# Kernel tuning notes

Measured on AMD Instinct MI355X. Metric: run time of the kernel, lower is better.

The kernel has to match this reference:

```python
import jax, jax.numpy as jnp
import numpy as np

TEMPERATURE = 0.07


def setup_inputs() -> dict:
    key = jax.random.key(0)
    k1, k2, k3 = jax.random.split(key, 3)
    b, num_proposals, num_phrases, f = 128, 100, 16, 512
    img_features = jax.random.normal(k1, (b, num_proposals, f), dtype=jnp.float32)
    text_features = jax.random.normal(k2, (b, num_phrases, f), dtype=jnp.float32)
    labels = jax.random.randint(k3, (b, b), 0, 2, dtype=jnp.int64)
    return {"img_features": img_features, "text_features": text_features, "labels": labels}


def reference(img_features, text_features, labels):
    # att_matrix[b,d,t,i] = <text[b,t,:], img[d,i,:]>
    att_matrix = jnp.einsum('btf,dif->bdti', text_features, img_features)
    argmax_box = att_matrix.max(axis=3)        # [b, d, t]  max over proposals
    score_matrix = argmax_box.mean(axis=2)     # [b, d]     mean over phrases
    score_exp = jnp.exp(score_matrix / TEMPERATURE)
    return score_exp
```

## Files before the change

kernel.cpp:

```cpp
#include <hip/hip_runtime.h>
#include <hip/hip_bf16.h>
#include <stdint.h>


typedef __attribute__((ext_vector_type(4))) int   v4i;
typedef __attribute__((ext_vector_type(8))) int   v8i;
typedef __attribute__((ext_vector_type(4))) float f32x4;

constexpr int Bb = 128;
constexpr int P  = 100;
constexpr int T  = 16;
constexpr int F  = 512;
constexpr float TEMP = 0.07f;

constexpr int BM = 128;
constexpr int BP = 112;
constexpr int BK = 128;
constexpr int NK = F / BK;
constexpr int NXCD = 8;

__global__ void cvt_kernel(const float4* __restrict__ img, const float4* __restrict__ txt,
                           uint32_t* __restrict__ imgb, uint32_t* __restrict__ txtb,
                           int nimg4, int ntxt4) {
  const int stride = gridDim.x * blockDim.x;
  for (int i = blockIdx.x * blockDim.x + threadIdx.x; i < nimg4; i += stride) {
    float4 v = img[i];
    int w = __builtin_amdgcn_cvt_pk_fp8_f32(v.x, v.y, 0, false);
    w     = __builtin_amdgcn_cvt_pk_fp8_f32(v.z, v.w, w, true);
    imgb[i] = (uint32_t)w;
  }
  for (int i = blockIdx.x * blockDim.x + threadIdx.x; i < ntxt4; i += stride) {
    float4 v = txt[i];
    int w = __builtin_amdgcn_cvt_pk_fp8_f32(v.x, v.y, 0, false);
    w     = __builtin_amdgcn_cvt_pk_fp8_f32(v.z, v.w, w, true);
    txtb[i] = (uint32_t)w;
  }
}

template<bool FUSED>
__global__ __launch_bounds__(256, 3)
void score_kernel(const void* __restrict__ imgp, const void* __restrict__ txtp,
                  float* __restrict__ out) {
  __shared__ __align__(16) unsigned char As[BM * BK];
  __shared__ __align__(16) unsigned char Bs[BP * BK];
  __shared__ float red[BM][2];

  const int L    = blockIdx.x;
  const int xcd  = L & (NXCD - 1);
  const int slot = L >> 3;
  const int d    = xcd * 16 + (slot >> 4);
  const int b0   = (slot & 15) * (BM / T);

  const int tid  = threadIdx.x;
  const int lane = tid & 63;
  const int w    = tid >> 6;
  const int q    = lane >> 4;
  const int n    = lane & 15;
  const int mh   = w & 1;
  const int nh   = w >> 1;

  f32x4 acc[4][4] = {};

  auto stage = [&](int kk) {
    if constexpr (!FUSED) {
      const uint8_t* gi = (const uint8_t*)imgp;
      const uint8_t* gt = (const uint8_t*)txtp;
      const int sub = lane >> 3;
      const int col = (((lane & 7) ^ sub) & 7) * 16;
      #pragma unroll
      for (int rr = 0; rr < 4; rr++) {
        const int c   = rr * 4 + w;
        const int row = c * 8 + sub;
        const uint8_t* ga = gt + (size_t)(b0 * T + row) * F + kk + col;
        __builtin_amdgcn_global_load_lds(
            (const __attribute__((address_space(1))) void*)ga,
            (__attribute__((address_space(3))) void*)&As[c * 1024], 16, 0, 0);
        if (c < BP / 8) {
          const int prow = row < P ? row : 0;
          const uint8_t* gb = gi + ((size_t)d * P + prow) * F + kk + col;
          __builtin_amdgcn_global_load_lds(
              (const __attribute__((address_space(1))) void*)gb,
              (__attribute__((address_space(3))) void*)&Bs[c * 1024], 16, 0, 0);
        }
      }
    } else {
      const float* gi = (const float*)imgp;
      const float* gt = (const float*)txtp;
      #pragma unroll
      for (int s = 0; s < 8; s++) {
        const int slot2 = s * 256 + tid;
        const int row   = slot2 >> 4;
        const int half  = slot2 & 15;
        const int colf  = half * 8;
        const int swz   = ((half >> 1) ^ (row & 7));
        const int offb  = row * BK + swz * 16 + (half & 1) * 8;
        float4 v0 = *(const float4*)(gt + (size_t)(b0 * T + row) * F + kk + colf);
        float4 v1 = *(const float4*)(gt + (size_t)(b0 * T + row) * F + kk + colf + 4);
        int w0 = __builtin_amdgcn_cvt_pk_fp8_f32(v0.x, v0.y, 0, false);
        w0     = __builtin_amdgcn_cvt_pk_fp8_f32(v0.z, v0.w, w0, true);
        int w1 = __builtin_amdgcn_cvt_pk_fp8_f32(v1.x, v1.y, 0, false);
        w1     = __builtin_amdgcn_cvt_pk_fp8_f32(v1.z, v1.w, w1, true);
        *(uint2*)&As[offb] = make_uint2((uint32_t)w0, (uint32_t)w1);
        if (row < BP) {
          const int prow = row < P ? row : 0;
          float4 u0 = *(const float4*)(gi + ((size_t)d * P + prow) * F + kk + colf);
          float4 u1 = *(const float4*)(gi + ((size_t)d * P + prow) * F + kk + colf + 4);
          int x0 = __builtin_amdgcn_cvt_pk_fp8_f32(u0.x, u0.y, 0, false);
          x0     = __builtin_amdgcn_cvt_pk_fp8_f32(u0.z, u0.w, x0, true);
          int x1 = __builtin_amdgcn_cvt_pk_fp8_f32(u1.x, u1.y, 0, false);
          x1     = __builtin_amdgcn_cvt_pk_fp8_f32(u1.z, u1.w, x1, true);
          *(uint2*)&Bs[offb] = make_uint2((uint32_t)x0, (uint32_t)x1);
        }
      }
    }
  };

  const int s0 = (2 * q) ^ (n & 7);
  const int NCT = (BP / 16) - nh * 4;

  #pragma unroll
  for (int k4 = 0; k4 < NK; k4++) {
    stage(k4 * BK);
    __syncthreads();

    v8i a[4];
    #pragma unroll
    for (int rt = 0; rt < 4; rt++) {
      const int off = (mh * 64 + rt * 16 + n) * BK;
      v4i lo = *(const v4i*)&As[off + s0 * 16];
      v4i hi = *(const v4i*)&As[off + (s0 ^ 1) * 16];
      a[rt] = __builtin_shufflevector(lo, hi, 0, 1, 2, 3, 4, 5, 6, 7);
    }
    #pragma unroll
    for (int ct = 0; ct < 4; ct++) {
      if (ct < NCT) {
        const int off = (nh * 64 + ct * 16 + n) * BK;
        v4i lo = *(const v4i*)&Bs[off + s0 * 16];
        v4i hi = *(const v4i*)&Bs[off + (s0 ^ 1) * 16];
        v8i bfr = __builtin_shufflevector(lo, hi, 0, 1, 2, 3, 4, 5, 6, 7);
        __builtin_amdgcn_s_setprio(1);
        #pragma unroll
        for (int rt = 0; rt < 4; rt++)
          acc[rt][ct] = __builtin_amdgcn_mfma_scale_f32_16x16x128_f8f6f4(
              a[rt], bfr, acc[rt][ct], 0, 0, 0, 127, 0, 127);
        __builtin_amdgcn_s_setprio(0);
      }
    }

    if (k4 + 1 < NK) __syncthreads();
  }

  #pragma unroll
  for (int rt = 0; rt < 4; rt++) {
    float m[4];
    #pragma unroll
    for (int r = 0; r < 4; r++) {
      float v = -3.0e38f;
      #pragma unroll
      for (int ct = 0; ct < 4; ct++) {
        const bool valid = (ct < NCT) && (nh * 64 + ct * 16 + n) < P;
        const float x = acc[rt][ct][r];
        v = valid ? fmaxf(v, x) : v;
      }
      #pragma unroll
      for (int off = 1; off < 16; off <<= 1)
        v = fmaxf(v, __shfl_xor(v, off));
      m[r] = v;
    }
    if (n == 0) {
      #pragma unroll
      for (int r = 0; r < 4; r++)
        red[mh * 64 + rt * 16 + q * 4 + r][nh] = m[r];
    }
  }
  __syncthreads();

  if (tid < BM / T) {
    float s = 0.f;
    #pragma unroll
    for (int t = 0; t < T; t++) {
      const int r = tid * T + t;
      s += fmaxf(red[r][0], red[r][1]);
    }
    const float arg = fminf(s * (1.0f / (T * TEMP)), 88.0f);
    out[(size_t)(b0 + tid) * Bb + d] = expf(arg);
  }
}

extern "C" void kernel_launch(void* const* d_in, const int* in_sizes, int n_in,
                              void* d_out, int out_size, void* d_ws, size_t ws_size,
                              hipStream_t stream) {
  const float* img = (const float*)d_in[0];
  const float* txt = (const float*)d_in[1];
  float* out = (float*)d_out;

  const size_t imgN = (size_t)Bb * P * F;
  const size_t txtN = (size_t)Bb * T * F;
  const size_t need = imgN + txtN;

  dim3 grid((Bb * Bb * T) / BM);
  if (ws_size >= need) {
    uint8_t* imgb = (uint8_t*)d_ws;
    uint8_t* txtb = imgb + imgN;
    cvt_kernel<<<2048, 256, 0, stream>>>((const float4*)img, (const float4*)txt,
                                         (uint32_t*)imgb, (uint32_t*)txtb,
                                         (int)(imgN / 4), (int)(txtN / 4));
    score_kernel<false><<<grid, 256, 0, stream>>>(imgb, txtb, out);
  } else {
    score_kernel<true><<<grid, 256, 0, stream>>>(img, txt, out);
  }
}
```

Baseline: 100.1 us.

## Double K tile to 256 bytes, halve barriers, use nontemporal conversion loads

Widens the K slice staged into shared memory from 128 to 256 fp8 bytes, so the score kernel runs two stage/compute rounds instead of four and needs fewer barriers. The LDS staging layout and swizzle are rewritten for the 256-byte rows, and the launch-bounds occupancy hint is dropped. The fp32-to-fp8 conversion kernel now uses nontemporal loads and stores. Shared memory per block roughly doubles, which can lower occupancy and limit latency hiding between blocks.

```diff
diff --git a/kernel.cpp b/kernel.cpp
--- a/kernel.cpp
+++ b/kernel.cpp
@@ -3,9 +3,10 @@
 #include <stdint.h>
 
 
-typedef __attribute__((ext_vector_type(4))) int   v4i;
-typedef __attribute__((ext_vector_type(8))) int   v8i;
-typedef __attribute__((ext_vector_type(4))) float f32x4;
+typedef __attribute__((ext_vector_type(4))) int    v4i;
+typedef __attribute__((ext_vector_type(8))) int    v8i;
+typedef __attribute__((ext_vector_type(4))) float  f32x4;
+typedef __attribute__((ext_vector_type(4))) float  f4raw;
 
 constexpr int Bb = 128;
 constexpr int P  = 100;
@@ -13,36 +14,37 @@
 constexpr int F  = 512;
 constexpr float TEMP = 0.07f;
 
-constexpr int BM = 128;
-constexpr int BP = 112;
-constexpr int BK = 128;
-constexpr int NK = F / BK;
+constexpr int BM  = 128;
+constexpr int BP  = 112;
+constexpr int BKB = 256;
 constexpr int NXCD = 8;
 
-__global__ void cvt_kernel(const float4* __restrict__ img, const float4* __restrict__ txt,
+__global__ void cvt_kernel(const float* __restrict__ img, const float* __restrict__ txt,
                            uint32_t* __restrict__ imgb, uint32_t* __restrict__ txtb,
                            int nimg4, int ntxt4) {
   const int stride = gridDim.x * blockDim.x;
+  const f4raw* gi = (const f4raw*)img;
+  const f4raw* gt = (const f4raw*)txt;
   for (int i = blockIdx.x * blockDim.x + threadIdx.x; i < nimg4; i += stride) {
-    float4 v = img[i];
+    f4raw v = __builtin_nontemporal_load(&gi[i]);
     int w = __builtin_amdgcn_cvt_pk_fp8_f32(v.x, v.y, 0, false);
     w     = __builtin_amdgcn_cvt_pk_fp8_f32(v.z, v.w, w, true);
-    imgb[i] = (uint32_t)w;
+    __builtin_nontemporal_store((uint32_t)w, &imgb[i]);
   }
   for (int i = blockIdx.x * blockDim.x + threadIdx.x; i < ntxt4; i += stride) {
-    float4 v = txt[i];
+    f4raw v = __builtin_nontemporal_load(&gt[i]);
     int w = __builtin_amdgcn_cvt_pk_fp8_f32(v.x, v.y, 0, false);
     w     = __builtin_amdgcn_cvt_pk_fp8_f32(v.z, v.w, w, true);
-    txtb[i] = (uint32_t)w;
+    __builtin_nontemporal_store((uint32_t)w, &txtb[i]);
   }
 }
 
 template<bool FUSED>
-__global__ __launch_bounds__(256, 3)
+__global__ __launch_bounds__(256)
 void score_kernel(const void* __restrict__ imgp, const void* __restrict__ txtp,
                   float* __restrict__ out) {
-  __shared__ __align__(16) unsigned char As[BM * BK];
-  __shared__ __align__(16) unsigned char Bs[BP * BK];
+  __shared__ __align__(16) unsigned char As[BM * BKB];
+  __shared__ __align__(16) unsigned char Bs[BP * BKB];
   __shared__ float red[BM][2];
 
   const int L    = blockIdx.x;
@@ -65,35 +67,41 @@
     if constexpr (!FUSED) {
       const uint8_t* gi = (const uint8_t*)imgp;
       const uint8_t* gt = (const uint8_t*)txtp;
-      const int sub = lane >> 3;
-      const int col = (((lane & 7) ^ sub) & 7) * 16;
-      #pragma unroll
-      for (int rr = 0; rr < 4; rr++) {
+      const int sub  = lane >> 4;
+      const int slt  = lane & 15;
+      #pragma unroll
+      for (int rr = 0; rr < 8; rr++) {
         const int c   = rr * 4 + w;
-        const int row = c * 8 + sub;
+        const int row = c * 4 + sub;
+        const int col = (slt ^ (row & 7)) * 16;
         const uint8_t* ga = gt + (size_t)(b0 * T + row) * F + kk + col;
         __builtin_amdgcn_global_load_lds(
             (const __attribute__((address_space(1))) void*)ga,
             (__attribute__((address_space(3))) void*)&As[c * 1024], 16, 0, 0);
-        if (c < BP / 8) {
-          const int prow = row < P ? row : 0;
-          const uint8_t* gb = gi + ((size_t)d * P + prow) * F + kk + col;
-          __builtin_amdgcn_global_load_lds(
-              (const __attribute__((address_space(1))) void*)gb,
-              (__attribute__((address_space(3))) void*)&Bs[c * 1024], 16, 0, 0);
-        }
+      }
+      #pragma unroll
+      for (int rr = 0; rr < 7; rr++) {
+        const int c   = rr * 4 + w;
+        const int row = c * 4 + sub;
+        const int prow = row < P ? row : 0;
+        const int col = (slt ^ (row & 7)) * 16;
+        const uint8_t* gb = gi + ((size_t)d * P + prow) * F + kk + col;
+        __builtin_amdgcn_global_load_lds(
+            (const __attribute__((address_space(1))) void*)gb,
+            (__attribute__((address_space(3))) void*)&Bs[c * 1024], 16, 0, 0);
       }
     } else {
       const float* gi = (const float*)imgp;
       const float* gt = (const float*)txtp;
       #pragma unroll
-      for (int s = 0; s < 8; s++) {
-        const int slot2 = s * 256 + tid;
-        const int row   = slot2 >> 4;
-        const int half  = slot2 & 15;
-        const int colf  = half * 8;
-        const int swz   = ((half >> 1) ^ (row & 7));
-        const int offb  = row * BK + swz * 16 + (half & 1) * 8;
+      for (int s = 0; s < 16; s++) {
+        const int u    = s * 256 + tid;
+        const int row  = u >> 5;
+        const int rem  = u & 31;
+        const int g    = rem >> 1;
+        const int half = rem & 1;
+        const int colf = g * 16 + half * 8;
+        const int offb = row * BKB + (g ^ (row & 7)) * 16 + half * 8;
         float4 v0 = *(const float4*)(gt + (size_t)(b0 * T + row) * F + kk + colf);
         float4 v1 = *(const float4*)(gt + (size_t)(b0 * T + row) * F + kk + colf + 4);
         int w0 = __builtin_amdgcn_cvt_pk_fp8_f32(v0.x, v0.y, 0, false);
@@ -101,32 +109,37 @@
         int w1 = __builtin_amdgcn_cvt_pk_fp8_f32(v1.x, v1.y, 0, false);
         w1     = __builtin_amdgcn_cvt_pk_fp8_f32(v1.z, v1.w, w1, true);
         *(uint2*)&As[offb] = make_uint2((uint32_t)w0, (uint32_t)w1);
-        if (row < BP) {
-          const int prow = row < P ? row : 0;
-          float4 u0 = *(const float4*)(gi + ((size_t)d * P + prow) * F + kk + colf);
-          float4 u1 = *(const float4*)(gi + ((size_t)d * P + prow) * F + kk + colf + 4);
-          int x0 = __builtin_amdgcn_cvt_pk_fp8_f32(u0.x, u0.y, 0, false);
-          x0     = __builtin_amdgcn_cvt_pk_fp8_f32(u0.z, u0.w, x0, true);
-          int x1 = __builtin_amdgcn_cvt_pk_fp8_f32(u1.x, u1.y, 0, false);
-          x1     = __builtin_amdgcn_cvt_pk_fp8_f32(u1.z, u1.w, x1, true);
-          *(uint2*)&Bs[offb] = make_uint2((uint32_t)x0, (uint32_t)x1);
-        }
+      }
+      #pragma unroll
+      for (int s = 0; s < 14; s++) {
+        const int u    = s * 256 + tid;
+        const int row  = u >> 5;
+        const int rem  = u & 31;
+        const int g    = rem >> 1;
+        const int half = rem & 1;
+        const int colf = g * 16 + half * 8;
+        const int offb = row * BKB + (g ^ (row & 7)) * 16 + half * 8;
+        const int prow = row < P ? row : 0;
+        float4 u0 = *(const float4*)(gi + ((size_t)d * P + prow) * F + kk + colf);
+        float4 u1 = *(const float4*)(gi + ((size_t)d * P + prow) * F + kk + colf + 4);
+        int x0 = __builtin_amdgcn_cvt_pk_fp8_f32(u0.x, u0.y, 0, false);
+        x0     = __builtin_amdgcn_cvt_pk_fp8_f32(u0.z, u0.w, x0, true);
+        int x1 = __builtin_amdgcn_cvt_pk_fp8_f32(u1.x, u1.y, 0, false);
+        x1     = __builtin_amdgcn_cvt_pk_fp8_f32(u1.z, u1.w, x1, true);
+        *(uint2*)&Bs[offb] = make_uint2((uint32_t)x0, (uint32_t)x1);
       }
     }
   };
 
-  const int s0 = (2 * q) ^ (n & 7);
   const int NCT = (BP / 16) - nh * 4;
 
-  #pragma unroll
-  for (int k4 = 0; k4 < NK; k4++) {
-    stage(k4 * BK);
-    __syncthreads();
-
+  auto compute = [&](int ksub) {
+    const int k7   = n & 7;
+    const int s0   = ksub * 8 + ((2 * q) ^ k7);
     v8i a[4];
     #pragma unroll
     for (int rt = 0; rt < 4; rt++) {
-      const int off = (mh * 64 + rt * 16 + n) * BK;
+      const int off = (mh * 64 + rt * 16 + n) * BKB;
       v4i lo = *(const v4i*)&As[off + s0 * 16];
       v4i hi = *(const v4i*)&As[off + (s0 ^ 1) * 16];
       a[rt] = __builtin_shufflevector(lo, hi, 0, 1, 2, 3, 4, 5, 6, 7);
@@ -134,7 +147,7 @@
     #pragma unroll
     for (int ct = 0; ct < 4; ct++) {
       if (ct < NCT) {
-        const int off = (nh * 64 + ct * 16 + n) * BK;
+        const int off = (nh * 64 + ct * 16 + n) * BKB;
         v4i lo = *(const v4i*)&Bs[off + s0 * 16];
         v4i hi = *(const v4i*)&Bs[off + (s0 ^ 1) * 16];
         v8i bfr = __builtin_shufflevector(lo, hi, 0, 1, 2, 3, 4, 5, 6, 7);
@@ -146,9 +159,17 @@
         __builtin_amdgcn_s_setprio(0);
       }
     }
-
-    if (k4 + 1 < NK) __syncthreads();
-  }
+  };
+
+  stage(0);
+  __syncthreads();
+  compute(0);
+  compute(1);
+  __syncthreads();
+  stage(BKB);
+  __syncthreads();
+  compute(0);
+  compute(1);
 
   #pragma unroll
   for (int rt = 0; rt < 4; rt++) {
@@ -202,7 +223,7 @@
   if (ws_size >= need) {
     uint8_t* imgb = (uint8_t*)d_ws;
     uint8_t* txtb = imgb + imgN;
-    cvt_kernel<<<2048, 256, 0, stream>>>((const float4*)img, (const float4*)txt,
+    cvt_kernel<<<2048, 256, 0, stream>>>(img, txt,
                                          (uint32_t*)imgb, (uint32_t*)txtb,
                                          (int)(imgN / 4), (int)(txtN / 4));
     score_kernel<false><<<grid, 256, 0, stream>>>(imgb, txtb, out);
```

New measurement: 108.6 us. +8.4%, slower.

## Load MFMA fragments directly from global memory instead of staging through LDS

Applied to the files above, without the earlier changes.

Removes the shared-memory A/B staging buffers and the per-K-step barriers. Each wave now loads its fp8 MFMA operand fragments straight from global memory (L2/L1) into registers. Occupancy hint is lowered from 3 to 2 blocks per CU. This removes LDS traffic and synchronisation, but every wave now issues redundant global loads for shared fragments and there is no explicit prefetch, so it leans on the cache.

```diff
diff --git a/kernel.cpp b/kernel.cpp
--- a/kernel.cpp
+++ b/kernel.cpp
@@ -3,9 +3,9 @@
 #include <stdint.h>
 
 
-typedef __attribute__((ext_vector_type(4))) int   v4i;
-typedef __attribute__((ext_vector_type(8))) int   v8i;
-typedef __attribute__((ext_vector_type(4))) float f32x4;
+typedef __attribute__((ext_vector_type(4))) int    v4i;
+typedef __attribute__((ext_vector_type(8))) int    v8i;
+typedef __attribute__((ext_vector_type(4))) float  f32x4;
 
 constexpr int Bb = 128;
 constexpr int P  = 100;
@@ -13,10 +13,7 @@
 constexpr int F  = 512;
 constexpr float TEMP = 0.07f;
 
-constexpr int BM = 128;
-constexpr int BP = 112;
-constexpr int BK = 128;
-constexpr int NK = F / BK;
+constexpr int BM  = 128;
 constexpr int NXCD = 8;
 
 __global__ void cvt_kernel(const float4* __restrict__ img, const float4* __restrict__ txt,
@@ -38,11 +35,9 @@
 }
 
 template<bool FUSED>
-__global__ __launch_bounds__(256, 3)
+__global__ __launch_bounds__(256, 2)
 void score_kernel(const void* __restrict__ imgp, const void* __restrict__ txtp,
                   float* __restrict__ out) {
-  __shared__ __align__(16) unsigned char As[BM * BK];
-  __shared__ __align__(16) unsigned char Bs[BP * BK];
   __shared__ float red[BM][2];
 
   const int L    = blockIdx.x;
@@ -58,96 +53,76 @@
   const int n    = lane & 15;
   const int mh   = w & 1;
   const int nh   = w >> 1;
+  const int NCT  = 4 - nh;
 
   f32x4 acc[4][4] = {};
 
-  auto stage = [&](int kk) {
+  auto frag8 = [](const uint8_t* p) -> v8i {
+    v4i lo = *(const v4i*)p;
+    v4i hi = *(const v4i*)(p + 16);
+    return __builtin_shufflevector(lo, hi, 0, 1, 2, 3, 4, 5, 6, 7);
+  };
+  auto frag32 = [](const float* p) -> v8i {
+    int wd[8];
+    #pragma unroll
+    for (int j = 0; j < 4; j++) {
+      float4 v0 = *(const float4*)(p + j * 8);
+      float4 v1 = *(const float4*)(p + j * 8 + 4);
+      int lo = __builtin_amdgcn_cvt_pk_fp8_f32(v0.x, v0.y, 0, false);
+      lo     = __builtin_amdgcn_cvt_pk_fp8_f32(v0.z, v0.w, lo, true);
+      int hi = __builtin_amdgcn_cvt_pk_fp8_f32(v1.x, v1.y, 0, false);
+      hi     = __builtin_amdgcn_cvt_pk_fp8_f32(v1.z, v1.w, hi, true);
+      wd[j * 2] = lo; wd[j * 2 + 1] = hi;
+    }
+    return v8i{wd[0], wd[1], wd[2], wd[3], wd[4], wd[5], wd[6], wd[7]};
+  };
+
+  int arow[4], brow[4];
+  #pragma unroll
+  for (int rt = 0; rt < 4; rt++) arow[rt] = b0 * T + mh * 64 + rt * 16 + n;
+  #pragma unroll
+  for (int ct = 0; ct < 4; ct++) {
+    const int col = nh * 64 + ct * 16 + n;
+    brow[ct] = (size_t)d * P + (col < P ? col : 0);
+  }
+
+  #pragma unroll
+  for (int k4 = 0; k4 < 4; k4++) {
+    const int koff = k4 * 128 + q * 32;
+    v8i a[4];
     if constexpr (!FUSED) {
+      const uint8_t* gt = (const uint8_t*)txtp;
+      #pragma unroll
+      for (int rt = 0; rt < 4; rt++)
+        a[rt] = frag8(gt + (size_t)arow[rt] * F + koff);
       const uint8_t* gi = (const uint8_t*)imgp;
-      const uint8_t* gt = (const uint8_t*)txtp;
-      const int sub = lane >> 3;
-      const int col = (((lane & 7) ^ sub) & 7) * 16;
       #pragma unroll
-      for (int rr = 0; rr < 4; rr++) {
-        const int c   = rr * 4 + w;
-        const int row = c * 8 + sub;
-        const uint8_t* ga = gt + (size_t)(b0 * T + row) * F + kk + col;
-        __builtin_amdgcn_global_load_lds(
-            (const __attribute__((address_space(1))) void*)ga,
-            (__attribute__((address_space(3))) void*)&As[c * 1024], 16, 0, 0);
-        if (c < BP / 8) {
-          const int prow = row < P ? row : 0;
-          const uint8_t* gb = gi + ((size_t)d * P + prow) * F + kk + col;
-          __builtin_amdgcn_global_load_lds(
-              (const __attribute__((address_space(1))) void*)gb,
-              (__attribute__((address_space(3))) void*)&Bs[c * 1024], 16, 0, 0);
+      for (int ct = 0; ct < 4; ct++) {
+        if (ct < NCT) {
+          v8i b = frag8(gi + (size_t)brow[ct] * F + koff);
+          #pragma unroll
+          for (int rt = 0; rt < 4; rt++)
+            acc[rt][ct] = __builtin_amdgcn_mfma_scale_f32_16x16x128_f8f6f4(
+                a[rt], b, acc[rt][ct], 0, 0, 0, 127, 0, 127);
         }
       }
     } else {
-      const float* gi = (const float*)imgp;
       const float* gt = (const float*)txtp;
       #pragma unroll
-      for (int s = 0; s < 8; s++) {
-        const int slot2 = s * 256 + tid;
-        const int row   = slot2 >> 4;
-        const int half  = slot2 & 15;
-        const int colf  = half * 8;
-        const int swz   = ((half >> 1) ^ (row & 7));
-        const int offb  = row * BK + swz * 16 + (half & 1) * 8;
-        float4 v0 = *(const float4*)(gt + (size_t)(b0 * T + row) * F + kk + colf);
-        float4 v1 = *(const float4*)(gt + (size_t)(b0 * T + row) * F + kk + colf + 4);
-        int w0 = __builtin_amdgcn_cvt_pk_fp8_f32(v0.x, v0.y, 0, false);
-        w0     = __builtin_amdgcn_cvt_pk_fp8_f32(v0.z, v0.w, w0, true);
-        int w1 = __builtin_amdgcn_cvt_pk_fp8_f32(v1.x, v1.y, 0, false);
-        w1     = __builtin_amdgcn_cvt_pk_fp8_f32(v1.z, v1.w, w1, true);
-        *(uint2*)&As[offb] = make_uint2((uint32_t)w0, (uint32_t)w1);
-        if (row < BP) {
-          const int prow = row < P ? row : 0;
-          float4 u0 = *(const float4*)(gi + ((size_t)d * P + prow) * F + kk + colf);
-          float4 u1 = *(const float4*)(gi + ((size_t)d * P + prow) * F + kk + colf + 4);
-          int x0 = __builtin_amdgcn_cvt_pk_fp8_f32(u0.x, u0.y, 0, false);
-          x0     = __builtin_amdgcn_cvt_pk_fp8_f32(u0.z, u0.w, x0, true);
-          int x1 = __builtin_amdgcn_cvt_pk_fp8_f32(u1.x, u1.y, 0, false);
-          x1     = __builtin_amdgcn_cvt_pk_fp8_f32(u1.z, u1.w, x1, true);
-          *(uint2*)&Bs[offb] = make_uint2((uint32_t)x0, (uint32_t)x1);
+      for (int rt = 0; rt < 4; rt++)
+        a[rt] = frag32(gt + (size_t)arow[rt] * F + koff);
+      const float* gi = (const float*)imgp;
+      #pragma unroll
+      for (int ct = 0; ct < 4; ct++) {
+        if (ct < NCT) {
+          v8i b = frag32(gi + (size_t)brow[ct] * F + koff);
+          #pragma unroll
+          for (int rt = 0; rt < 4; rt++)
+            acc[rt][ct] = __builtin_amdgcn_mfma_scale_f32_16x16x128_f8f6f4(
+                a[rt], b, acc[rt][ct], 0, 0, 0, 127, 0, 127);
         }
       }
     }
-  };
-
-  const int s0 = (2 * q) ^ (n & 7);
-  const int NCT = (BP / 16) - nh * 4;
-
-  #pragma unroll
-  for (int k4 = 0; k4 < NK; k4++) {
-    stage(k4 * BK);
-    __syncthreads();
-
-    v8i a[4];
-    #pragma unroll
-    for (int rt = 0; rt < 4; rt++) {
-      const int off = (mh * 64 + rt * 16 + n) * BK;
-      v4i lo = *(const v4i*)&As[off + s0 * 16];
-      v4i hi = *(const v4i*)&As[off + (s0 ^ 1) * 16];
-      a[rt] = __builtin_shufflevector(lo, hi, 0, 1, 2, 3, 4, 5, 6, 7);
-    }
-    #pragma unroll
-    for (int ct = 0; ct < 4; ct++) {
-      if (ct < NCT) {
-        const int off = (nh * 64 + ct * 16 + n) * BK;
-        v4i lo = *(const v4i*)&Bs[off + s0 * 16];
-        v4i hi = *(const v4i*)&Bs[off + (s0 ^ 1) * 16];
-        v8i bfr = __builtin_shufflevector(lo, hi, 0, 1, 2, 3, 4, 5, 6, 7);
-        __builtin_amdgcn_s_setprio(1);
-        #pragma unroll
-        for (int rt = 0; rt < 4; rt++)
-          acc[rt][ct] = __builtin_amdgcn_mfma_scale_f32_16x16x128_f8f6f4(
-              a[rt], bfr, acc[rt][ct], 0, 0, 0, 127, 0, 127);
-        __builtin_amdgcn_s_setprio(0);
-      }
-    }
-
-    if (k4 + 1 < NK) __syncthreads();
   }
 
   #pragma unroll
```

Result: slower. 131.3 us (+31.1%).
